# Kernel optimization log

Measured on AMD Instinct MI355X. Metric: run time of the kernel, lower is better.

## Reference

```python
import jax, jax.numpy as jnp
import numpy as np

N = 100000
E = 1600000
IN_C, HID, OUT_C = 128, 128, 64
NUM_LAYERS = 3


def setup_inputs() -> dict:
    key = jax.random.key(0)
    ks = jax.random.split(key, 8)
    x = jax.random.normal(ks[0], (N, IN_C), dtype=jnp.float32)
    edge_index = jax.random.randint(ks[1], (2, E), 0, N, dtype=jnp.int64)
    s_in = 1.0 / np.sqrt(IN_C)
    s_h = 1.0 / np.sqrt(HID)
    W_in = jax.random.uniform(ks[2], (IN_C, HID), jnp.float32, -s_in, s_in)
    b_in = jax.random.uniform(ks[3], (HID,), jnp.float32, -s_in, s_in)
    conv_W = jax.random.uniform(ks[4], (NUM_LAYERS, HID, HID), jnp.float32, -s_h, s_h)
    conv_b = jnp.zeros((NUM_LAYERS, HID), jnp.float32)
    W_out = jax.random.uniform(ks[5], (HID, OUT_C), jnp.float32, -s_h, s_h)
    b_out = jax.random.uniform(ks[6], (OUT_C,), jnp.float32, -s_h, s_h)
    return {"x": x, "edge_index": edge_index, "W_in": W_in, "b_in": b_in,
            "conv_W": conv_W, "conv_b": conv_b, "W_out": W_out, "b_out": b_out}


def reference(x, edge_index, W_in, b_in, conv_W, conv_b, W_out, b_out):
    n = x.shape[0]
    loops = jnp.arange(n, dtype=edge_index.dtype)
    # add self-loops (PyG GCNConv default)
    rows = jnp.concatenate([edge_index[0], loops])  # source nodes
    cols = jnp.concatenate([edge_index[1], loops])  # target nodes
    deg = jax.ops.segment_sum(jnp.ones_like(cols, dtype=x.dtype), cols, num_segments=n)
    dinv = jnp.where(deg > 0, jax.lax.rsqrt(deg), 0.0)
    norm = (dinv[rows] * dinv[cols])[:, None]  # [E+N, 1] symmetric normalization

    def gcn_conv(h, W, b):
        h = h @ W  # [N, HID]
        msg = h[rows] * norm  # gather + scale, [E+N, HID]
        return jax.ops.segment_sum(msg, cols, num_segments=n) + b

    h = jax.nn.relu(x @ W_in + b_in)
    for l in range(conv_W.shape[0]):
        h = jax.nn.relu(gcn_conv(h, conv_W[l], conv_b[l]))
    logits = h @ W_out + b_out
    return logits
```

## Files before the change

### kernel.cpp

```cpp
#include <hip/hip_runtime.h>

typedef __attribute__((ext_vector_type(8))) short short8;
typedef __attribute__((ext_vector_type(4))) float f32x4;

#define NPB   128
#define CAPB  2688
#define TILE  8192
#define MAXB  800

__device__ __forceinline__ float bfLO(unsigned u){
  union { unsigned x; float f; } c; c.x = u << 16; return c.f;
}
__device__ __forceinline__ float bfHI(unsigned u){
  union { unsigned x; float f; } c; c.x = u & 0xffff0000u; return c.f;
}
__device__ __forceinline__ unsigned short f2bf(float f){
  union { float f; unsigned u; } v; v.f = f;
  unsigned r = v.u + 0x7fffu + ((v.u >> 16) & 1u);
  return (unsigned short)(r >> 16);
}

__global__ void k_wprep_all(const float* __restrict__ W_in, const float* __restrict__ convW,
                            const float* __restrict__ W_out, unsigned short* __restrict__ Bf,
                            int* __restrict__ zeroPtr, int zeroN){
  if (blockIdx.x >= 40){
    int i = (blockIdx.x - 40)*256 + threadIdx.x;
    if (i < zeroN) zeroPtr[i] = 0;
    return;
  }
  const int slot = blockIdx.x >> 3;
  const int idx  = (blockIdx.x & 7)*256 + threadIdx.x;
  const float* W; int ncol;
  if (slot == 0){ W = W_in; ncol = 128; }
  else if (slot <= 3){ W = convW + (size_t)(slot-1)*128*128; ncol = 128; }
  else { W = W_out; ncol = 64; }
  const int l = idx & 63, ks = (idx >> 6) & 3, cb = idx >> 8;
  if (cb >= (ncol >> 4)) return;
  const int c  = cb*16 + (l & 15);
  const int k0 = ks*32 + ((l >> 4) << 3);
  unsigned short* o = Bf + (size_t)slot*16384 + (size_t)idx*8;
#pragma unroll
  for (int j = 0; j < 8; ++j) o[j] = f2bf(W[(size_t)(k0 + j)*ncol + c]);
}

__global__ __launch_bounds__(256) void k_bucket2(const void* ei,
    int* __restrict__ bcnt, unsigned* __restrict__ buf, int E, int nbuck)
{
  __shared__ unsigned recs[TILE];
  __shared__ unsigned short recb[TILE];
  __shared__ int cnt[MAXB];
  __shared__ int offs[MAXB];
  __shared__ int ofc[MAXB];
  __shared__ int gbase[MAXB];
  __shared__ int sc[256];
  __shared__ int s_i64;

  const int tid = threadIdx.x;
  if (tid < 64){
    unsigned v = ((const unsigned*)ei)[2*tid + 1];
    unsigned long long any = __ballot(v != 0u);
    if (tid == 0) s_i64 = (any == 0ull) ? 1 : 0;
  }
  const int e0 = blockIdx.x * TILE;
  const int m = min(TILE, E - e0);
  if (m <= 0) return;

  for (int i = tid; i < nbuck; i += 256) cnt[i] = 0;
  __syncthreads();
  const bool i64 = s_i64 != 0;

  for (int i = tid; i < m; i += 256){
    int c = i64 ? (int)((const long long*)ei)[(size_t)E + e0 + i]
                : ((const int*)ei)[(size_t)E + e0 + i];
    atomicAdd(&cnt[c >> 7], 1);
  }
  __syncthreads();

  int lc[4]; int tsum = 0;
#pragma unroll
  for (int j = 0; j < 4; ++j){
    int b = tid*4 + j;
    lc[j] = (b < nbuck) ? cnt[b] : 0;
    tsum += lc[j];
  }
  sc[tid] = tsum; __syncthreads();
  for (int off = 1; off < 256; off <<= 1){
    int a = (tid >= off) ? sc[tid - off] : 0;
    __syncthreads(); sc[tid] += a; __syncthreads();
  }
  int run = sc[tid] - tsum;
#pragma unroll
  for (int j = 0; j < 4; ++j){
    int b = tid*4 + j;
    if (b < nbuck){
      offs[b] = run; ofc[b] = run;
      gbase[b] = lc[j] ? atomicAdd(&bcnt[b*16], lc[j]) : 0;
    }
    run += lc[j];
  }
  __syncthreads();

  for (int i = tid; i < m; i += 256){
    int r, c;
    if (i64){ const long long* p = (const long long*)ei; r = (int)p[e0+i]; c = (int)p[(size_t)E+e0+i]; }
    else    { const int* p = (const int*)ei;            r = p[e0+i];      c = p[(size_t)E+e0+i]; }
    int b = c >> 7;
    int pos = atomicAdd(&ofc[b], 1);
    recs[pos] = ((unsigned)(c & (NPB-1)) << 17) | (unsigned)r;
    recb[pos] = (unsigned short)b;
  }
  __syncthreads();

  for (int i = tid; i < m; i += 256){
    int b = recb[i];
    int dst = gbase[b] + (i - offs[b]);
    if (dst < CAPB) buf[(size_t)b*CAPB + dst] = recs[i];
  }
}

__global__ __launch_bounds__(256) void k_csr2(const int* __restrict__ bcnt,
    const unsigned* __restrict__ buf, int2* __restrict__ nspan,
    int* __restrict__ srcl, float* __restrict__ dinv, int* __restrict__ cursor, int N){
  __shared__ unsigned recs[CAPB];
  __shared__ int cnt[NPB];
  __shared__ int ex[NPB];
  __shared__ int sc[256];
  __shared__ int s_base;
  const int b = blockIdx.x, tid = threadIdx.x;
  const int m = min(bcnt[b*16], CAPB);
  if (tid == 0) s_base = atomicAdd(cursor, m);

  if (tid < NPB) cnt[tid] = 0;
  __syncthreads();
  for (int i = tid; i < m; i += 256){
    unsigned rec = buf[(size_t)b*CAPB + i];
    recs[i] = rec;
    atomicAdd(&cnt[rec >> 17], 1);
  }
  __syncthreads();
  const int base = s_base;
  int v = (tid < NPB) ? cnt[tid] : 0;
  sc[tid] = v; __syncthreads();
  for (int off = 1; off < 256; off <<= 1){
    int a = (tid >= off) ? sc[tid - off] : 0;
    __syncthreads();
    sc[tid] += a;
    __syncthreads();
  }
  if (tid < NPB){
    int excl = sc[tid] - v;
    ex[tid] = excl;
    int g = b*NPB + tid;
    if (g < N){
      nspan[g] = make_int2(base + excl, v);
      dinv[g]  = rsqrtf((float)v + 1.0f);
    }
  }
  __syncthreads();
  for (int i = tid; i < m; i += 256){
    unsigned rec = recs[i];
    int pos = base + atomicAdd(&ex[rec >> 17], 1);
    srcl[pos] = (int)(rec & 0x1FFFFu);
  }
}

template<int NCOL, bool A_F32, bool BIAS, bool RELU, bool SCALE, bool OUT_F32>
__global__ __launch_bounds__(256) void k_mm(const void* __restrict__ Ap,
    const unsigned short* __restrict__ Bf, const float* __restrict__ bias,
    const float* __restrict__ dinv, void* __restrict__ Cp, int nrows)
{
  constexpr int NCB = NCOL/16;
  const int tid = threadIdx.x;
  const int wave = tid >> 6, l = tid & 63;
  const int lr = l & 15, lg = l >> 4;
  const int row0 = blockIdx.x*128 + wave*32;

  f32x4 acc[2][NCB];
#pragma unroll
  for (int i = 0; i < 2; ++i)
#pragma unroll
    for (int j = 0; j < NCB; ++j) acc[i][j] = f32x4{0.f, 0.f, 0.f, 0.f};

  const int r0 = row0 + lr, r1 = row0 + 16 + lr;
  const bool ok0 = r0 < nrows, ok1 = r1 < nrows;

#pragma unroll
  for (int ks = 0; ks < 4; ++ks){
    const int kbase = ks*32 + lg*8;
    short8 a0 = short8{0,0,0,0,0,0,0,0}, a1 = short8{0,0,0,0,0,0,0,0};
    if constexpr (A_F32){
      const float* A = (const float*)Ap;
      if (ok0){
        const float* p = A + (size_t)r0*128 + kbase;
        f32x4 x0 = *(const f32x4*)p, x1 = *(const f32x4*)(p + 4);
#pragma unroll
        for (int j = 0; j < 4; ++j){ a0[j] = (short)f2bf(x0[j]); a0[j+4] = (short)f2bf(x1[j]); }
      }
      if (ok1){
        const float* p = A + (size_t)r1*128 + kbase;
        f32x4 x0 = *(const f32x4*)p, x1 = *(const f32x4*)(p + 4);
#pragma unroll
        for (int j = 0; j < 4; ++j){ a1[j] = (short)f2bf(x0[j]); a1[j+4] = (short)f2bf(x1[j]); }
      }
    } else {
      const unsigned short* A = (const unsigned short*)Ap;
      if (ok0) a0 = *(const short8*)(A + (size_t)r0*128 + kbase);
      if (ok1) a1 = *(const short8*)(A + (size_t)r1*128 + kbase);
    }
#pragma unroll
    for (int cb = 0; cb < NCB; ++cb){
      short8 b = *(const short8*)(Bf + ((size_t)(cb*4 + ks)*64 + l)*8);
      acc[0][cb] = __builtin_amdgcn_mfma_f32_16x16x32_bf16(a0, b, acc[0][cb], 0, 0, 0);
      acc[1][cb] = __builtin_amdgcn_mfma_f32_16x16x32_bf16(a1, b, acc[1][cb], 0, 0, 0);
    }
  }

#pragma unroll
  for (int rb = 0; rb < 2; ++rb){
#pragma unroll
    for (int j = 0; j < 4; ++j){
      const int r = row0 + rb*16 + lg*4 + j;
      if (r >= nrows) continue;
      const float dv = SCALE ? dinv[r] : 1.0f;
#pragma unroll
      for (int cb = 0; cb < NCB; ++cb){
        const int c = cb*16 + lr;
        float v = acc[rb][cb][j];
        if constexpr (BIAS) v += bias[c];
        if constexpr (RELU) v = fmaxf(v, 0.0f);
        if constexpr (SCALE) v *= dv;
        if constexpr (OUT_F32) ((float*)Cp)[(size_t)r*NCOL + c] = v;
        else ((unsigned short*)Cp)[(size_t)r*NCOL + c] = f2bf(v);
      }
    }
  }
}

__global__ __launch_bounds__(256, 8) void k_agg(const unsigned* __restrict__ t,
    const int2* __restrict__ nspan, const int* __restrict__ srcl,
    const float* __restrict__ dinv, const float* __restrict__ bias,
    unsigned* __restrict__ hout, int n)
{
  const int node = blockIdx.x*4 + (threadIdx.x >> 6);
  if (node >= n) return;
  const int l = threadIdx.x & 63;

  const int2 sp = nspan[node];
  int i = sp.x;
  const int e = sp.x + sp.y;

  unsigned v = t[(size_t)node*64 + l];
  float a0 = bfLO(v), a1 = bfHI(v);

  int idx = (i < e) ? srcl[min(i + l, e - 1)] : 0;
  while (i < e){
    const int cnt = min(e - i, 64);
    const int nexti = i + cnt;
    const int idxn = (nexti < e) ? srcl[min(nexti + l, e - 1)] : 0;
    int j = 0;
    for (; j + 16 <= cnt; j += 16){
      unsigned u[16];
#pragma unroll
      for (int q = 0; q < 16; ++q){
        int s = __builtin_amdgcn_readlane(idx, j + q);
        u[q] = t[(size_t)s*64 + l];
      }
#pragma unroll
      for (int q = 0; q < 16; ++q){ a0 += bfLO(u[q]); a1 += bfHI(u[q]); }
    }
    for (; j + 8 <= cnt; j += 8){
      unsigned u[8];
#pragma unroll
      for (int q = 0; q < 8; ++q){
        int s = __builtin_amdgcn_readlane(idx, j + q);
        u[q] = t[(size_t)s*64 + l];
      }
#pragma unroll
      for (int q = 0; q < 8; ++q){ a0 += bfLO(u[q]); a1 += bfHI(u[q]); }
    }
    for (; j + 4 <= cnt; j += 4){
      unsigned u[4];
#pragma unroll
      for (int q = 0; q < 4; ++q){
        int s = __builtin_amdgcn_readlane(idx, j + q);
        u[q] = t[(size_t)s*64 + l];
      }
#pragma unroll
      for (int q = 0; q < 4; ++q){ a0 += bfLO(u[q]); a1 += bfHI(u[q]); }
    }
    for (; j < cnt; ++j){
      int s = __builtin_amdgcn_readlane(idx, j);
      unsigned u0 = t[(size_t)s*64 + l];
      a0 += bfLO(u0); a1 += bfHI(u0);
    }
    i = nexti; idx = idxn;
  }
  const float d = dinv[node];
  float o0 = fmaxf(fmaf(d, a0, bias[2*l]),     0.0f);
  float o1 = fmaxf(fmaf(d, a1, bias[2*l + 1]), 0.0f);
  hout[(size_t)node*64 + l] = (unsigned)f2bf(o0) | ((unsigned)f2bf(o1) << 16);
}

extern "C" void kernel_launch(void* const* d_in, const int* in_sizes, int n_in,
                              void* d_out, int out_size, void* d_ws, size_t ws_size,
                              hipStream_t stream)
{
  const float* x     = (const float*)d_in[0];
  const void*  ei    = d_in[1];
  const float* W_in  = (const float*)d_in[2];
  const float* b_in  = (const float*)d_in[3];
  const float* convW = (const float*)d_in[4];
  const float* convb = (const float*)d_in[5];
  const float* W_out = (const float*)d_in[6];
  const float* b_out = (const float*)d_in[7];
  float* out = (float*)d_out;

  const int N = in_sizes[0] / 128;
  const int E = in_sizes[1] / 2;
  const int NBUCK = (N + NPB - 1) / NPB;

  char* w = (char*)d_ws;
  auto alloc = [&](size_t b){ char* p = w; w += (b + 255) & ~(size_t)255; return p; };
  unsigned short* h    = (unsigned short*)alloc((size_t)N*128*2);
  unsigned short* t    = (unsigned short*)alloc((size_t)N*128*2);
  unsigned short* Bf   = (unsigned short*)alloc((size_t)5*16384*2);
  float* dinv          = (float*)alloc((size_t)N*4);
  int2* nspan          = (int2*)alloc((size_t)N*8);
  int* srcl            = (int*)alloc((size_t)E*4);
  int* bcnt            = (int*)alloc((size_t)(NBUCK*16 + 16)*4);
  unsigned* bbuf       = (unsigned*)t;

  int* cursor = bcnt + NBUCK*16;
  const int zeroN = NBUCK*16 + 16;
  const int ZB = (zeroN + 255)/256;
  const int MB = (N + 127) / 128;

  k_wprep_all<<<40 + ZB, 256, 0, stream>>>(W_in, convW, W_out, Bf, bcnt, zeroN);
  k_bucket2<<<(E + TILE - 1)/TILE, 256, 0, stream>>>(ei, bcnt, bbuf, E, NBUCK);
  k_csr2  <<<NBUCK, 256, 0, stream>>>(bcnt, bbuf, nspan, srcl, dinv, cursor, N);

  k_mm<128, true, true, true, false, false><<<MB, 256, 0, stream>>>(x, Bf, b_in, nullptr, h, N);

  for (int L = 0; L < 3; ++L){
    k_mm<128, false, false, false, true, false><<<MB, 256, 0, stream>>>(h, Bf + (size_t)(1+L)*16384, nullptr, dinv, t, N);
    k_agg<<<(N + 3)/4, 256, 0, stream>>>((const unsigned*)t, nspan, srcl, dinv,
                                         convb + (size_t)L*128, (unsigned*)h, N);
  }

  k_mm<64, false, true, false, false, true><<<MB, 256, 0, stream>>>(h, Bf + (size_t)4*16384, b_out, nullptr, out, N);
}
```

Baseline: 345.3 us.

## Fuse aggregation with following GEMM via aggregate-then-transform reordering

Reorders each GCN layer to aggregate first and then multiply by W, so the aggregation result for a 128-node tile stays in LDS and feeds MFMA directly in one kernel. The dinv prescale moves into the previous GEMM epilogue, and the final output projection is fused into the last conv kernel. This removes the separate per-layer GEMM launches and their intermediate global round trips. In exchange, each block processes 128 nodes serially per wave (32 per wave), which lowers the parallelism available to the latency-bound gather. The 32 KB LDS per block and the dropped occupancy hint may also reduce occupancy.

Result: slower. 574.3 us (+66.3%).

```diff
diff --git a/kernel.cpp b/kernel.cpp
--- a/kernel.cpp
+++ b/kernel.cpp
@@ -236,69 +236,164 @@
   }
 }
 
-__global__ __launch_bounds__(256, 8) void k_agg(const unsigned* __restrict__ t,
+template<bool LAST>
+__global__ __launch_bounds__(256) void k_conv(const unsigned* __restrict__ hs,
     const int2* __restrict__ nspan, const int* __restrict__ srcl,
-    const float* __restrict__ dinv, const float* __restrict__ bias,
-    unsigned* __restrict__ hout, int n)
+    const float* __restrict__ dinv, const unsigned short* __restrict__ Bf,
+    const float* __restrict__ bias, const unsigned short* __restrict__ BfO,
+    const float* __restrict__ bias_out, void* __restrict__ outp, int n)
 {
-  const int node = blockIdx.x*4 + (threadIdx.x >> 6);
-  if (node >= n) return;
-  const int l = threadIdx.x & 63;
-
-  const int2 sp = nspan[node];
-  int i = sp.x;
-  const int e = sp.x + sp.y;
-
-  unsigned v = t[(size_t)node*64 + l];
-  float a0 = bfLO(v), a1 = bfHI(v);
-
-  int idx = (i < e) ? srcl[min(i + l, e - 1)] : 0;
-  while (i < e){
-    const int cnt = min(e - i, 64);
-    const int nexti = i + cnt;
-    const int idxn = (nexti < e) ? srcl[min(nexti + l, e - 1)] : 0;
-    int j = 0;
-    for (; j + 16 <= cnt; j += 16){
-      unsigned u[16];
-#pragma unroll
-      for (int q = 0; q < 16; ++q){
-        int s = __builtin_amdgcn_readlane(idx, j + q);
-        u[q] = t[(size_t)s*64 + l];
-      }
-#pragma unroll
-      for (int q = 0; q < 16; ++q){ a0 += bfLO(u[q]); a1 += bfHI(u[q]); }
-    }
-    for (; j + 8 <= cnt; j += 8){
-      unsigned u[8];
-#pragma unroll
-      for (int q = 0; q < 8; ++q){
-        int s = __builtin_amdgcn_readlane(idx, j + q);
-        u[q] = t[(size_t)s*64 + l];
-      }
-#pragma unroll
-      for (int q = 0; q < 8; ++q){ a0 += bfLO(u[q]); a1 += bfHI(u[q]); }
-    }
-    for (; j + 4 <= cnt; j += 4){
-      unsigned u[4];
-#pragma unroll
-      for (int q = 0; q < 4; ++q){
-        int s = __builtin_amdgcn_readlane(idx, j + q);
-        u[q] = t[(size_t)s*64 + l];
-      }
-#pragma unroll
-      for (int q = 0; q < 4; ++q){ a0 += bfLO(u[q]); a1 += bfHI(u[q]); }
-    }
-    for (; j < cnt; ++j){
-      int s = __builtin_amdgcn_readlane(idx, j);
-      unsigned u0 = t[(size_t)s*64 + l];
-      a0 += bfLO(u0); a1 += bfHI(u0);
-    }
-    i = nexti; idx = idxn;
-  }
-  const float d = dinv[node];
-  float o0 = fmaxf(fmaf(d, a0, bias[2*l]),     0.0f);
-  float o1 = fmaxf(fmaf(d, a1, bias[2*l + 1]), 0.0f);
-  hout[(size_t)node*64 + l] = (unsigned)f2bf(o0) | ((unsigned)f2bf(o1) << 16);
+  __shared__ char u_raw[128*256];
+  const int tid = threadIdx.x, wave = tid >> 6, l = tid & 63;
+  const int lr = l & 15, lg = l >> 4;
+
+  for (int nn = 0; nn < 32; ++nn){
+    const int node = blockIdx.x*128 + wave*32 + nn;
+    if (node >= n) continue;
+    const int2 sp = nspan[node];
+    int i = sp.x;
+    const int e = sp.x + sp.y;
+
+    unsigned v = hs[(size_t)node*64 + l];
+    float a0 = bfLO(v), a1 = bfHI(v);
+
+    int idx = (i < e) ? srcl[min(i + l, e - 1)] : 0;
+    while (i < e){
+      const int cnt = min(e - i, 64);
+      const int nexti = i + cnt;
+      const int idxn = (nexti < e) ? srcl[min(nexti + l, e - 1)] : 0;
+      int j = 0;
+      for (; j + 16 <= cnt; j += 16){
+        unsigned u[16];
+#pragma unroll
+        for (int q = 0; q < 16; ++q){
+          int s = __builtin_amdgcn_readlane(idx, j + q);
+          u[q] = hs[(size_t)s*64 + l];
+        }
+#pragma unroll
+        for (int q = 0; q < 16; ++q){ a0 += bfLO(u[q]); a1 += bfHI(u[q]); }
+      }
+      for (; j + 8 <= cnt; j += 8){
+        unsigned u[8];
+#pragma unroll
+        for (int q = 0; q < 8; ++q){
+          int s = __builtin_amdgcn_readlane(idx, j + q);
+          u[q] = hs[(size_t)s*64 + l];
+        }
+#pragma unroll
+        for (int q = 0; q < 8; ++q){ a0 += bfLO(u[q]); a1 += bfHI(u[q]); }
+      }
+      for (; j + 4 <= cnt; j += 4){
+        unsigned u[4];
+#pragma unroll
+        for (int q = 0; q < 4; ++q){
+          int s = __builtin_amdgcn_readlane(idx, j + q);
+          u[q] = hs[(size_t)s*64 + l];
+        }
+#pragma unroll
+        for (int q = 0; q < 4; ++q){ a0 += bfLO(u[q]); a1 += bfHI(u[q]); }
+      }
+      for (; j < cnt; ++j){
+        int s = __builtin_amdgcn_readlane(idx, j);
+        unsigned u0 = hs[(size_t)s*64 + l];
+        a0 += bfLO(u0); a1 += bfHI(u0);
+      }
+      i = nexti; idx = idxn;
+    }
+    const float dv = dinv[node];
+    const int lrow = wave*32 + nn;
+    unsigned pk = (unsigned)f2bf(dv*a0) | ((unsigned)f2bf(dv*a1) << 16);
+    *(unsigned*)(u_raw + ((lrow*256 + l*4) ^ ((lrow & 7) << 4))) = pk;
+  }
+  __syncthreads();
+
+  f32x4 acc[2][8];
+#pragma unroll
+  for (int i = 0; i < 2; ++i)
+#pragma unroll
+    for (int j = 0; j < 8; ++j) acc[i][j] = f32x4{0.f, 0.f, 0.f, 0.f};
+
+  const int r0l = wave*32 + lr, r1l = r0l + 16;
+#pragma unroll
+  for (int ks = 0; ks < 4; ++ks){
+    const int off = ks*64 + lg*16;
+    short8 a0 = *(const short8*)(u_raw + ((r0l*256 + off) ^ ((r0l & 7) << 4)));
+    short8 a1 = *(const short8*)(u_raw + ((r1l*256 + off) ^ ((r1l & 7) << 4)));
+#pragma unroll
+    for (int cb = 0; cb < 8; ++cb){
+      short8 b = *(const short8*)(Bf + ((size_t)(cb*4 + ks)*64 + l)*8);
+      acc[0][cb] = __builtin_amdgcn_mfma_f32_16x16x32_bf16(a0, b, acc[0][cb], 0, 0, 0);
+      acc[1][cb] = __builtin_amdgcn_mfma_f32_16x16x32_bf16(a1, b, acc[1][cb], 0, 0, 0);
+    }
+  }
+
+  if constexpr (!LAST){
+    unsigned short* H = (unsigned short*)outp;
+#pragma unroll
+    for (int rb = 0; rb < 2; ++rb){
+#pragma unroll
+      for (int j = 0; j < 4; ++j){
+        const int r = blockIdx.x*128 + wave*32 + rb*16 + lg*4 + j;
+        if (r >= n) continue;
+        const float dv = dinv[r];
+#pragma unroll
+        for (int cb = 0; cb < 8; ++cb){
+          const int c = cb*16 + lr;
+          float v = fmaxf(acc[rb][cb][j] + bias[c], 0.0f) * dv;
+          H[(size_t)r*128 + c] = f2bf(v);
+        }
+      }
+    }
+  } else {
+    __syncthreads();
+#pragma unroll
+    for (int rb = 0; rb < 2; ++rb){
+#pragma unroll
+      for (int j = 0; j < 4; ++j){
+        const int lrow = wave*32 + rb*16 + lg*4 + j;
+#pragma unroll
+        for (int cb = 0; cb < 8; ++cb){
+          const int c = cb*16 + lr;
+          float v = fmaxf(acc[rb][cb][j] + bias[c], 0.0f);
+          *(unsigned short*)(u_raw + ((lrow*256 + c*2) ^ ((lrow & 7) << 4))) = f2bf(v);
+        }
+      }
+    }
+    __syncthreads();
+
+    f32x4 acc2[2][4];
+#pragma unroll
+    for (int i = 0; i < 2; ++i)
+#pragma unroll
+      for (int j = 0; j < 4; ++j) acc2[i][j] = f32x4{0.f, 0.f, 0.f, 0.f};
+
+#pragma unroll
+    for (int ks = 0; ks < 4; ++ks){
+      const int off = ks*64 + lg*16;
+      short8 a0 = *(const short8*)(u_raw + ((r0l*256 + off) ^ ((r0l & 7) << 4)));
+      short8 a1 = *(const short8*)(u_raw + ((r1l*256 + off) ^ ((r1l & 7) << 4)));
+#pragma unroll
+      for (int cb = 0; cb < 4; ++cb){
+        short8 b = *(const short8*)(BfO + ((size_t)(cb*4 + ks)*64 + l)*8);
+        acc2[0][cb] = __builtin_amdgcn_mfma_f32_16x16x32_bf16(a0, b, acc2[0][cb], 0, 0, 0);
+        acc2[1][cb] = __builtin_amdgcn_mfma_f32_16x16x32_bf16(a1, b, acc2[1][cb], 0, 0, 0);
+      }
+    }
+    float* O = (float*)outp;
+#pragma unroll
+    for (int rb = 0; rb < 2; ++rb){
+#pragma unroll
+      for (int j = 0; j < 4; ++j){
+        const int r = blockIdx.x*128 + wave*32 + rb*16 + lg*4 + j;
+        if (r >= n) continue;
+#pragma unroll
+        for (int cb = 0; cb < 4; ++cb){
+          const int c = cb*16 + lr;
+          O[(size_t)r*64 + c] = acc2[rb][cb][j] + bias_out[c];
+        }
+      }
+    }
+  }
 }
 
 extern "C" void kernel_launch(void* const* d_in, const int* in_sizes, int n_in,
@@ -339,13 +434,12 @@
   k_bucket2<<<(E + TILE - 1)/TILE, 256, 0, stream>>>(ei, bcnt, bbuf, E, NBUCK);
   k_csr2  <<<NBUCK, 256, 0, stream>>>(bcnt, bbuf, nspan, srcl, dinv, cursor, N);
 
-  k_mm<128, true, true, true, false, false><<<MB, 256, 0, stream>>>(x, Bf, b_in, nullptr, h, N);
-
-  for (int L = 0; L < 3; ++L){
-    k_mm<128, false, false, false, true, false><<<MB, 256, 0, stream>>>(h, Bf + (size_t)(1+L)*16384, nullptr, dinv, t, N);
-    k_agg<<<(N + 3)/4, 256, 0, stream>>>((const unsigned*)t, nspan, srcl, dinv,
-                                         convb + (size_t)L*128, (unsigned*)h, N);
-  }
-
-  k_mm<64, false, true, false, false, true><<<MB, 256, 0, stream>>>(h, Bf + (size_t)4*16384, b_out, nullptr, out, N);
-}
+  k_mm<128, true, true, true, true, false><<<MB, 256, 0, stream>>>(x, Bf, b_in, dinv, h, N);
+
+  k_conv<false><<<MB, 256, 0, stream>>>((const unsigned*)h, nspan, srcl, dinv,
+      Bf + (size_t)1*16384, convb + 0*128, nullptr, nullptr, t, N);
+  k_conv<false><<<MB, 256, 0, stream>>>((const unsigned*)t, nspan, srcl, dinv,
+      Bf + (size_t)2*16384, convb + 1*128, nullptr, nullptr, h, N);
+  k_conv<true><<<MB, 256, 0, stream>>>((const unsigned*)h, nspan, srcl, dinv,
+      Bf + (size_t)3*16384, convb + 2*128, Bf + (size_t)4*16384, b_out, out, N);
+}
```

## Fuse CSR build with first matmuls in combined kernels and move dinv scaling

Applied to the files above, without the earlier changes.

The input matmul now runs in the same launch as edge bucketing, and the first conv matmul in the same launch as CSR construction, so independent work overlaps and there are fewer launches. The bucket buffer moves to the output allocation so it no longer aliases t. The dinv row scaling leaves the matmul epilogue. Layer 0 aggregation applies dinv per source through an extra gather, and the aggregation epilogue pre-scales h by dinv for the next layer. The edge tile size is halved to give more bucketing blocks, which costs extra per-block overhead and more fragmented bucket writes.

Result: faster. 309.6 us (-10.3%).

```diff
diff --git a/kernel.cpp b/kernel.cpp
--- a/kernel.cpp
+++ b/kernel.cpp
@@ -5,7 +5,7 @@
 
 #define NPB   128
 #define CAPB  2688
-#define TILE  8192
+#define TILE  4096
 #define MAXB  800
 
 __device__ __forceinline__ float bfLO(unsigned u){
@@ -43,7 +43,84 @@
   for (int j = 0; j < 8; ++j) o[j] = f2bf(W[(size_t)(k0 + j)*ncol + c]);
 }
 
-__global__ __launch_bounds__(256) void k_bucket2(const void* ei,
+template<int NCOL, bool A_F32, bool BIAS, bool RELU, bool OUT_F32>
+__device__ __forceinline__ void mm_body(int bid, const void* __restrict__ Ap,
+    const unsigned short* __restrict__ Bf, const float* __restrict__ bias,
+    void* __restrict__ Cp, int nrows)
+{
+  constexpr int NCB = NCOL/16;
+  const int tid = threadIdx.x;
+  const int wave = tid >> 6, l = tid & 63;
+  const int lr = l & 15, lg = l >> 4;
+  const int row0 = bid*128 + wave*32;
+
+  f32x4 acc[2][NCB];
+#pragma unroll
+  for (int i = 0; i < 2; ++i)
+#pragma unroll
+    for (int j = 0; j < NCB; ++j) acc[i][j] = f32x4{0.f, 0.f, 0.f, 0.f};
+
+  const int r0 = row0 + lr, r1 = row0 + 16 + lr;
+  const bool ok0 = r0 < nrows, ok1 = r1 < nrows;
+
+#pragma unroll
+  for (int ks = 0; ks < 4; ++ks){
+    const int kbase = ks*32 + lg*8;
+    short8 a0 = short8{0,0,0,0,0,0,0,0}, a1 = short8{0,0,0,0,0,0,0,0};
+    if constexpr (A_F32){
+      const float* A = (const float*)Ap;
+      if (ok0){
+        const float* p = A + (size_t)r0*128 + kbase;
+        f32x4 x0 = *(const f32x4*)p, x1 = *(const f32x4*)(p + 4);
+#pragma unroll
+        for (int j = 0; j < 4; ++j){ a0[j] = (short)f2bf(x0[j]); a0[j+4] = (short)f2bf(x1[j]); }
+      }
+      if (ok1){
+        const float* p = A + (size_t)r1*128 + kbase;
+        f32x4 x0 = *(const f32x4*)p, x1 = *(const f32x4*)(p + 4);
+#pragma unroll
+        for (int j = 0; j < 4; ++j){ a1[j] = (short)f2bf(x0[j]); a1[j+4] = (short)f2bf(x1[j]); }
+      }
+    } else {
+      const unsigned short* A = (const unsigned short*)Ap;
+      if (ok0) a0 = *(const short8*)(A + (size_t)r0*128 + kbase);
+      if (ok1) a1 = *(const short8*)(A + (size_t)r1*128 + kbase);
+    }
+#pragma unroll
+    for (int cb = 0; cb < NCB; ++cb){
+      short8 b = *(const short8*)(Bf + ((size_t)(cb*4 + ks)*64 + l)*8);
+      acc[0][cb] = __builtin_amdgcn_mfma_f32_16x16x32_bf16(a0, b, acc[0][cb], 0, 0, 0);
+      acc[1][cb] = __builtin_amdgcn_mfma_f32_16x16x32_bf16(a1, b, acc[1][cb], 0, 0, 0);
+    }
+  }
+
+#pragma unroll
+  for (int rb = 0; rb < 2; ++rb){
+#pragma unroll
+    for (int j = 0; j < 4; ++j){
+      const int r = row0 + rb*16 + lg*4 + j;
+      if (r >= nrows) continue;
+#pragma unroll
+      for (int cb = 0; cb < NCB; ++cb){
+        const int c = cb*16 + lr;
+        float v = acc[rb][cb][j];
+        if constexpr (BIAS) v += bias[c];
+        if constexpr (RELU) v = fmaxf(v, 0.0f);
+        if constexpr (OUT_F32) ((float*)Cp)[(size_t)r*NCOL + c] = v;
+        else ((unsigned short*)Cp)[(size_t)r*NCOL + c] = f2bf(v);
+      }
+    }
+  }
+}
+
+template<int NCOL, bool A_F32, bool BIAS, bool RELU, bool OUT_F32>
+__global__ __launch_bounds__(256) void k_mm_g(const void* __restrict__ Ap,
+    const unsigned short* __restrict__ Bf, const float* __restrict__ bias,
+    void* __restrict__ Cp, int nrows){
+  mm_body<NCOL, A_F32, BIAS, RELU, OUT_F32>(blockIdx.x, Ap, Bf, bias, Cp, nrows);
+}
+
+__device__ __forceinline__ void bucket2_body(int bid, const void* ei,
     int* __restrict__ bcnt, unsigned* __restrict__ buf, int E, int nbuck)
 {
   __shared__ unsigned recs[TILE];
@@ -61,7 +138,7 @@
     unsigned long long any = __ballot(v != 0u);
     if (tid == 0) s_i64 = (any == 0ull) ? 1 : 0;
   }
-  const int e0 = blockIdx.x * TILE;
+  const int e0 = bid * TILE;
   const int m = min(TILE, E - e0);
   if (m <= 0) return;
 
@@ -118,15 +195,16 @@
   }
 }
 
-__global__ __launch_bounds__(256) void k_csr2(const int* __restrict__ bcnt,
+__device__ __forceinline__ void csr2_body(int b, const int* __restrict__ bcnt,
     const unsigned* __restrict__ buf, int2* __restrict__ nspan,
-    int* __restrict__ srcl, float* __restrict__ dinv, int* __restrict__ cursor, int N){
+    int* __restrict__ srcl, float* __restrict__ dinv, int* __restrict__ cursor, int N)
+{
   __shared__ unsigned recs[CAPB];
   __shared__ int cnt[NPB];
   __shared__ int ex[NPB];
   __shared__ int sc[256];
   __shared__ int s_base;
-  const int b = blockIdx.x, tid = threadIdx.x;
+  const int tid = threadIdx.x;
   const int m = min(bcnt[b*16], CAPB);
   if (tid == 0) s_base = atomicAdd(cursor, m);
 
@@ -164,78 +242,30 @@
   }
 }
 
-template<int NCOL, bool A_F32, bool BIAS, bool RELU, bool SCALE, bool OUT_F32>
-__global__ __launch_bounds__(256) void k_mm(const void* __restrict__ Ap,
-    const unsigned short* __restrict__ Bf, const float* __restrict__ bias,
-    const float* __restrict__ dinv, void* __restrict__ Cp, int nrows)
-{
-  constexpr int NCB = NCOL/16;
-  const int tid = threadIdx.x;
-  const int wave = tid >> 6, l = tid & 63;
-  const int lr = l & 15, lg = l >> 4;
-  const int row0 = blockIdx.x*128 + wave*32;
-
-  f32x4 acc[2][NCB];
-#pragma unroll
-  for (int i = 0; i < 2; ++i)
-#pragma unroll
-    for (int j = 0; j < NCB; ++j) acc[i][j] = f32x4{0.f, 0.f, 0.f, 0.f};
-
-  const int r0 = row0 + lr, r1 = row0 + 16 + lr;
-  const bool ok0 = r0 < nrows, ok1 = r1 < nrows;
-
-#pragma unroll
-  for (int ks = 0; ks < 4; ++ks){
-    const int kbase = ks*32 + lg*8;
-    short8 a0 = short8{0,0,0,0,0,0,0,0}, a1 = short8{0,0,0,0,0,0,0,0};
-    if constexpr (A_F32){
-      const float* A = (const float*)Ap;
-      if (ok0){
-        const float* p = A + (size_t)r0*128 + kbase;
-        f32x4 x0 = *(const f32x4*)p, x1 = *(const f32x4*)(p + 4);
-#pragma unroll
-        for (int j = 0; j < 4; ++j){ a0[j] = (short)f2bf(x0[j]); a0[j+4] = (short)f2bf(x1[j]); }
-      }
-      if (ok1){
-        const float* p = A + (size_t)r1*128 + kbase;
-        f32x4 x0 = *(const f32x4*)p, x1 = *(const f32x4*)(p + 4);
-#pragma unroll
-        for (int j = 0; j < 4; ++j){ a1[j] = (short)f2bf(x0[j]); a1[j+4] = (short)f2bf(x1[j]); }
-      }
-    } else {
-      const unsigned short* A = (const unsigned short*)Ap;
-      if (ok0) a0 = *(const short8*)(A + (size_t)r0*128 + kbase);
-      if (ok1) a1 = *(const short8*)(A + (size_t)r1*128 + kbase);
-    }
-#pragma unroll
-    for (int cb = 0; cb < NCB; ++cb){
-      short8 b = *(const short8*)(Bf + ((size_t)(cb*4 + ks)*64 + l)*8);
-      acc[0][cb] = __builtin_amdgcn_mfma_f32_16x16x32_bf16(a0, b, acc[0][cb], 0, 0, 0);
-      acc[1][cb] = __builtin_amdgcn_mfma_f32_16x16x32_bf16(a1, b, acc[1][cb], 0, 0, 0);
-    }
-  }
-
-#pragma unroll
-  for (int rb = 0; rb < 2; ++rb){
-#pragma unroll
-    for (int j = 0; j < 4; ++j){
-      const int r = row0 + rb*16 + lg*4 + j;
-      if (r >= nrows) continue;
-      const float dv = SCALE ? dinv[r] : 1.0f;
-#pragma unroll
-      for (int cb = 0; cb < NCB; ++cb){
-        const int c = cb*16 + lr;
-        float v = acc[rb][cb][j];
-        if constexpr (BIAS) v += bias[c];
-        if constexpr (RELU) v = fmaxf(v, 0.0f);
-        if constexpr (SCALE) v *= dv;
-        if constexpr (OUT_F32) ((float*)Cp)[(size_t)r*NCOL + c] = v;
-        else ((unsigned short*)Cp)[(size_t)r*NCOL + c] = f2bf(v);
-      }
-    }
-  }
-}
-
+__global__ __launch_bounds__(256, 4) void k_fat1(const float* __restrict__ x,
+    const unsigned short* __restrict__ Bf, const float* __restrict__ b_in,
+    unsigned short* __restrict__ h, const void* ei, int* __restrict__ bcnt,
+    unsigned* __restrict__ bbuf, int E, int nbuck, int N, int MB)
+{
+  if ((int)blockIdx.x < MB)
+    mm_body<128, true, true, true, false>(blockIdx.x, x, Bf, b_in, h, N);
+  else
+    bucket2_body(blockIdx.x - MB, ei, bcnt, bbuf, E, nbuck);
+}
+
+__global__ __launch_bounds__(256, 4) void k_fat2(const unsigned short* __restrict__ h,
+    const unsigned short* __restrict__ Bf1, unsigned short* __restrict__ t,
+    const int* __restrict__ bcnt, const unsigned* __restrict__ bbuf,
+    int2* __restrict__ nspan, int* __restrict__ srcl, float* __restrict__ dinv,
+    int* __restrict__ cursor, int N, int MB)
+{
+  if ((int)blockIdx.x < MB)
+    mm_body<128, false, false, false, false>(blockIdx.x, h, Bf1, nullptr, t, N);
+  else
+    csr2_body(blockIdx.x - MB, bcnt, bbuf, nspan, srcl, dinv, cursor, N);
+}
+
+template<bool SCALED, bool HNEXT>
 __global__ __launch_bounds__(256, 8) void k_agg(const unsigned* __restrict__ t,
     const int2* __restrict__ nspan, const int* __restrict__ srcl,
     const float* __restrict__ dinv, const float* __restrict__ bias,
@@ -248,56 +278,102 @@
   const int2 sp = nspan[node];
   int i = sp.x;
   const int e = sp.x + sp.y;
+  const float dvc = dinv[node];
 
   unsigned v = t[(size_t)node*64 + l];
-  float a0 = bfLO(v), a1 = bfHI(v);
-
-  int idx = (i < e) ? srcl[min(i + l, e - 1)] : 0;
-  while (i < e){
-    const int cnt = min(e - i, 64);
-    const int nexti = i + cnt;
-    const int idxn = (nexti < e) ? srcl[min(nexti + l, e - 1)] : 0;
-    int j = 0;
-    for (; j + 16 <= cnt; j += 16){
-      unsigned u[16];
-#pragma unroll
-      for (int q = 0; q < 16; ++q){
-        int s = __builtin_amdgcn_readlane(idx, j + q);
-        u[q] = t[(size_t)s*64 + l];
-      }
-#pragma unroll
-      for (int q = 0; q < 16; ++q){ a0 += bfLO(u[q]); a1 += bfHI(u[q]); }
-    }
-    for (; j + 8 <= cnt; j += 8){
-      unsigned u[8];
-#pragma unroll
-      for (int q = 0; q < 8; ++q){
-        int s = __builtin_amdgcn_readlane(idx, j + q);
-        u[q] = t[(size_t)s*64 + l];
-      }
-#pragma unroll
-      for (int q = 0; q < 8; ++q){ a0 += bfLO(u[q]); a1 += bfHI(u[q]); }
-    }
-    for (; j + 4 <= cnt; j += 4){
-      unsigned u[4];
-#pragma unroll
-      for (int q = 0; q < 4; ++q){
-        int s = __builtin_amdgcn_readlane(idx, j + q);
-        u[q] = t[(size_t)s*64 + l];
-      }
-#pragma unroll
-      for (int q = 0; q < 4; ++q){ a0 += bfLO(u[q]); a1 += bfHI(u[q]); }
-    }
-    for (; j < cnt; ++j){
-      int s = __builtin_amdgcn_readlane(idx, j);
-      unsigned u0 = t[(size_t)s*64 + l];
-      a0 += bfLO(u0); a1 += bfHI(u0);
-    }
-    i = nexti; idx = idxn;
-  }
-  const float d = dinv[node];
-  float o0 = fmaxf(fmaf(d, a0, bias[2*l]),     0.0f);
-  float o1 = fmaxf(fmaf(d, a1, bias[2*l + 1]), 0.0f);
+  float a0, a1;
+  if constexpr (SCALED){ a0 = dvc*bfLO(v); a1 = dvc*bfHI(v); }
+  else                 { a0 = bfLO(v);     a1 = bfHI(v); }
+
+  if constexpr (SCALED){
+    int idx = (i < e) ? srcl[min(i + l, e - 1)] : 0;
+    while (i < e){
+      const int cnt = min(e - i, 64);
+      const int nexti = i + cnt;
+      const int idxn = (nexti < e) ? srcl[min(nexti + l, e - 1)] : 0;
+      int j = 0;
+      for (; j + 8 <= cnt; j += 8){
+        int sv[8]; unsigned u[8]; float dv[8];
+#pragma unroll
+        for (int q = 0; q < 8; ++q) sv[q] = __shfl(idx, j + q);
+#pragma unroll
+        for (int q = 0; q < 8; ++q){ u[q] = t[(size_t)sv[q]*64 + l]; dv[q] = dinv[sv[q]]; }
+#pragma unroll
+        for (int q = 0; q < 8; ++q){
+          a0 = fmaf(dv[q], bfLO(u[q]), a0);
+          a1 = fmaf(dv[q], bfHI(u[q]), a1);
+        }
+      }
+      for (; j + 4 <= cnt; j += 4){
+        int sv[4]; unsigned u[4]; float dv[4];
+#pragma unroll
+        for (int q = 0; q < 4; ++q) sv[q] = __shfl(idx, j + q);
+#pragma unroll
+        for (int q = 0; q < 4; ++q){ u[q] = t[(size_t)sv[q]*64 + l]; dv[q] = dinv[sv[q]]; }
+#pragma unroll
+        for (int q = 0; q < 4; ++q){
+          a0 = fmaf(dv[q], bfLO(u[q]), a0);
+          a1 = fmaf(dv[q], bfHI(u[q]), a1);
+        }
+      }
+      for (; j < cnt; ++j){
+        int s = __shfl(idx, j);
+        unsigned u0 = t[(size_t)s*64 + l];
+        float dv0 = dinv[s];
+        a0 = fmaf(dv0, bfLO(u0), a0);
+        a1 = fmaf(dv0, bfHI(u0), a1);
+      }
+      i = nexti; idx = idxn;
+    }
+  } else {
+    int idx = (i < e) ? srcl[min(i + l, e - 1)] : 0;
+    while (i < e){
+      const int cnt = min(e - i, 64);
+      const int nexti = i + cnt;
+      const int idxn = (nexti < e) ? srcl[min(nexti + l, e - 1)] : 0;
+      int j = 0;
+      for (; j + 16 <= cnt; j += 16){
+        unsigned u[16];
+#pragma unroll
+        for (int q = 0; q < 16; ++q){
+          int s = __builtin_amdgcn_readlane(idx, j + q);
+          u[q] = t[(size_t)s*64 + l];
+        }
+#pragma unroll
+        for (int q = 0; q < 16; ++q){ a0 += bfLO(u[q]); a1 += bfHI(u[q]); }
+      }
+      for (; j + 8 <= cnt; j += 8){
+        unsigned u[8];
+#pragma unroll
+        for (int q = 0; q < 8; ++q){
+          int s = __builtin_amdgcn_readlane(idx, j + q);
+          u[q] = t[(size_t)s*64 + l];
+        }
+#pragma unroll
+        for (int q = 0; q < 8; ++q){ a0 += bfLO(u[q]); a1 += bfHI(u[q]); }
+      }
+      for (; j + 4 <= cnt; j += 4){
+        unsigned u[4];
+#pragma unroll
+        for (int q = 0; q < 4; ++q){
+          int s = __builtin_amdgcn_readlane(idx, j + q);
+          u[q] = t[(size_t)s*64 + l];
+        }
+#pragma unroll
+        for (int q = 0; q < 4; ++q){ a0 += bfLO(u[q]); a1 += bfHI(u[q]); }
+      }
+      for (; j < cnt; ++j){
+        int s = __builtin_amdgcn_readlane(idx, j);
+        unsigned u0 = t[(size_t)s*64 + l];
+        a0 += bfLO(u0); a1 += bfHI(u0);
+      }
+      i = nexti; idx = idxn;
+    }
+  }
+
+  float o0 = fmaxf(fmaf(dvc, a0, bias[2*l]),     0.0f);
+  float o1 = fmaxf(fmaf(dvc, a1, bias[2*l + 1]), 0.0f);
+  if constexpr (HNEXT){ o0 *= dvc; o1 *= dvc; }
   hout[(size_t)node*64 + l] = (unsigned)f2bf(o0) | ((unsigned)f2bf(o1) << 16);
 }
 
@@ -328,24 +404,25 @@
   int2* nspan          = (int2*)alloc((size_t)N*8);
   int* srcl            = (int*)alloc((size_t)E*4);
   int* bcnt            = (int*)alloc((size_t)(NBUCK*16 + 16)*4);
-  unsigned* bbuf       = (unsigned*)t;
+  unsigned* bbuf       = (unsigned*)d_out;
 
   int* cursor = bcnt + NBUCK*16;
   const int zeroN = NBUCK*16 + 16;
   const int ZB = (zeroN + 255)/256;
   const int MB = (N + 127) / 128;
+  const int NB2 = (E + TILE - 1)/TILE;
 
   k_wprep_all<<<40 + ZB, 256, 0, stream>>>(W_in, convW, W_out, Bf, bcnt, zeroN);
-  k_bucket2<<<(E + TILE - 1)/TILE, 256, 0, stream>>>(ei, bcnt, bbuf, E, NBUCK);
-  k_csr2  <<<NBUCK, 256, 0, stream>>>(bcnt, bbuf, nspan, srcl, dinv, cursor, N);
-
-  k_mm<128, true, true, true, false, false><<<MB, 256, 0, stream>>>(x, Bf, b_in, nullptr, h, N);
-
-  for (int L = 0; L < 3; ++L){
-    k_mm<128, false, false, false, true, false><<<MB, 256, 0, stream>>>(h, Bf + (size_t)(1+L)*16384, nullptr, dinv, t, N);
-    k_agg<<<(N + 3)/4, 256, 0, stream>>>((const unsigned*)t, nspan, srcl, dinv,
-                                         convb + (size_t)L*128, (unsigned*)h, N);
-  }
-
-  k_mm<64, false, true, false, false, true><<<MB, 256, 0, stream>>>(h, Bf + (size_t)4*16384, b_out, nullptr, out, N);
-}
+  k_fat1<<<MB + NB2, 256, 0, stream>>>(x, Bf, b_in, h, ei, bcnt, bbuf, E, NBUCK, N, MB);
+  k_fat2<<<MB + NBUCK, 256, 0, stream>>>(h, Bf + (size_t)1*16384, t, bcnt, bbuf,
+                                         nspan, srcl, dinv, cursor, N, MB);
+  k_agg<true, true><<<(N + 3)/4, 256, 0, stream>>>((const unsigned*)t, nspan, srcl, dinv,
+                                                   convb + 0*128, (unsigned*)h, N);
+  k_mm_g<128, false, false, false, false><<<MB, 256, 0, stream>>>(h, Bf + (size_t)2*16384, nullptr, t, N);
+  k_agg<false, true><<<(N + 3)/4, 256, 0, stream>>>((const unsigned*)t, nspan, srcl, dinv,
+                                                    convb + 1*128, (unsigned*)h, N);
+  k_mm_g<128, false, false, false, false><<<MB, 256, 0, stream>>>(h, Bf + (size_t)3*16384, nullptr, t, N);
+  k_agg<false, false><<<(N + 3)/4, 256, 0, stream>>>((const unsigned*)t, nspan, srcl, dinv,
+                                                     convb + 2*128, (unsigned*)h, N);
+  k_mm_g<64, false, true, false, true><<<MB, 256, 0, stream>>>(h, Bf + (size_t)4*16384, b_out, out, N);
+}
```
